# Kernel tuning notes

Hardware: AMD Instinct MI355X
Metric: run time of the kernel (lower is better)

## Reference

```python
import jax, jax.numpy as jnp
import numpy as np


def setup_inputs() -> dict:
    key = jax.random.key(0)
    ks = jax.random.split(key, 7)
    B, T, I, H, O = 128, 1024, 300, 128, 64
    s_ih = 1.0 / np.sqrt(H)
    return {
        "x": jax.random.normal(ks[0], (B, T, I), dtype=jnp.float32),
        "W_ih": jax.random.normal(ks[1], (4 * H, I), dtype=jnp.float32) * s_ih,
        "W_hh": jax.random.normal(ks[2], (4 * H, H), dtype=jnp.float32) * s_ih,
        "b_ih": jax.random.normal(ks[3], (4 * H,), dtype=jnp.float32) * s_ih,
        "b_hh": jax.random.normal(ks[4], (4 * H,), dtype=jnp.float32) * s_ih,
        "W1": jax.random.normal(ks[5], (O, H), dtype=jnp.float32) * s_ih,
        "b1": jax.random.normal(ks[6], (O,), dtype=jnp.float32) * s_ih,
    }


def reference(x, W_ih, W_hh, b_ih, b_hh, W1, b1):
    B, T, I = x.shape
    H = W_hh.shape[1]
    # Precompute the input-to-gate projections for all timesteps at once: [B,T,4H]
    x_gates = jnp.einsum("bti,gi->btg", x, W_ih) + b_ih + b_hh

    def step(carry, xg_t):
        h, c = carry
        gates = xg_t + h @ W_hh.T  # [B, 4H]
        i_g, f_g, g_g, o_g = jnp.split(gates, 4, axis=-1)
        i_g = jax.nn.sigmoid(i_g)
        f_g = jax.nn.sigmoid(f_g)
        g_g = jnp.tanh(g_g)
        o_g = jax.nn.sigmoid(o_g)
        c_new = f_g * c + i_g * g_g
        h_new = o_g * jnp.tanh(c_new)
        return (h_new, c_new), h_new

    h0 = jnp.zeros((B, H), dtype=x.dtype)
    c0 = jnp.zeros((B, H), dtype=x.dtype)
    _, all_h = jax.lax.scan(step, (h0, c0), jnp.swapaxes(x_gates, 0, 1))  # [T,B,H]
    h_seq = jnp.swapaxes(all_h, 0, 1)  # [B,T,H]
    # Dropout in eval mode (identity) for a deterministic reference.
    y = jnp.einsum("bth,oh->bto", h_seq, W1) + b1
    return y
```

## Files before the change

### kernel.cpp

```cpp
#include <hip/hip_runtime.h>
#include <hip/hip_fp16.h>

typedef __attribute__((ext_vector_type(8))) short  s16x8;
typedef __attribute__((ext_vector_type(4))) float  f32x4;
typedef __attribute__((ext_vector_type(4))) unsigned short u16x4;
typedef _Float16 f16x2 __attribute__((ext_vector_type(2)));
typedef _Float16 f16x8 __attribute__((ext_vector_type(8)));
typedef unsigned short u16;

#define MFMA16B(A, B, C) __builtin_amdgcn_mfma_f32_16x16x32_bf16((A), (B), (C), 0, 0, 0)
#define MFMA16H(A, B, C) __builtin_amdgcn_mfma_f32_16x16x32_f16((A), (B), (C), 0, 0, 0)

static __device__ __forceinline__ u16 f2bf(float f) {
    union { float f; unsigned u; } v; v.f = f;
    unsigned r = (v.u + 0x7fffu + ((v.u >> 16) & 1u)) >> 16;
    return (u16)r;
}

static __device__ __forceinline__ s16x8 pack_f16x8(float4 a, float4 b) {
    s16x8 r;
    r[0] = (short)__half_as_ushort(__float2half_rn(a.x));
    r[1] = (short)__half_as_ushort(__float2half_rn(a.y));
    r[2] = (short)__half_as_ushort(__float2half_rn(a.z));
    r[3] = (short)__half_as_ushort(__float2half_rn(a.w));
    r[4] = (short)__half_as_ushort(__float2half_rn(b.x));
    r[5] = (short)__half_as_ushort(__float2half_rn(b.y));
    r[6] = (short)__half_as_ushort(__float2half_rn(b.z));
    r[7] = (short)__half_as_ushort(__float2half_rn(b.w));
    return r;
}

static __device__ __forceinline__ float hu2f(u16 v) {
    __half_raw hr; hr.x = v; return __half2float(__half(hr));
}

static __device__ __forceinline__ float sigm(float x) {
    return __builtin_amdgcn_rcpf(1.f + __expf(-x));
}
static __device__ __forceinline__ float tanh_f(float x) {
    float e = __expf(-2.f * x);
    return fmaf(2.f, __builtin_amdgcn_rcpf(1.f + e), -1.f);
}

static __device__ __forceinline__ void wg_barrier() {
    asm volatile("s_waitcnt lgkmcnt(0)\n\ts_barrier" ::: "memory");
}

static __device__ __forceinline__ void lds_fence() {
    asm volatile("s_waitcnt lgkmcnt(0)" ::: "memory");
}

#define DPPB(v, ctrl) __builtin_bit_cast(float, __builtin_amdgcn_update_dpp(    \
        0, __builtin_bit_cast(int, (v)), (ctrl), 0xf, 0xf, true))

__global__ __launch_bounds__(256, 2)
void k1_gemm_xgates(const float* __restrict__ x, const float* __restrict__ W_ih,
                    const float* __restrict__ b_ih, const float* __restrict__ b_hh,
                    __half* __restrict__ xg) {
    const int n0 = blockIdx.x * 128;
    const int m0 = blockIdx.y * 128;
    const int tid = threadIdx.x;
    const int wave = tid >> 6, lane = tid & 63;
    const int lanelo = lane & 15, quad = lane >> 4;
    const int mw = (wave & 1) * 64, nw = (wave >> 1) * 64;

    __shared__ __align__(16) u16 As[128 * 40];
    __shared__ __align__(16) u16 Bs[128 * 40];

    f32x4 acc[4][4];
#pragma unroll
    for (int i = 0; i < 4; ++i)
#pragma unroll
        for (int j = 0; j < 4; ++j) acc[i][j] = (f32x4)0.f;

    const int srow = tid >> 1;
    const int scol = (tid & 1) * 16;
    const int grow = (srow & 3) * 128 + (n0 >> 2) + (srow >> 2);

    for (int kc = 0; kc < 10; ++kc) {
        const int k0 = kc * 32;
        const float* srcA = x + (size_t)(m0 + srow) * 300 + k0 + scol;
        const float* srcB = W_ih + (size_t)grow * 300 + k0 + scol;
        if (kc < 9) {
#pragma unroll
            for (int i = 0; i < 4; ++i) {
                const int col = scol + i * 4;
                float4 v = *(const float4*)(srcA + i * 4);
                u16x4 w; w.x = f2bf(v.x); w.y = f2bf(v.y); w.z = f2bf(v.z); w.w = f2bf(v.w);
                *(u16x4*)&As[srow * 40 + col] = w;
                float4 u = *(const float4*)(srcB + i * 4);
                u16x4 q; q.x = f2bf(u.x); q.y = f2bf(u.y); q.z = f2bf(u.z); q.w = f2bf(u.w);
                *(u16x4*)&Bs[srow * 40 + col] = q;
            }
        } else {
#pragma unroll
            for (int i = 0; i < 4; ++i) {
                const int col = scol + i * 4;
                float4 v = {0.f, 0.f, 0.f, 0.f}, u = {0.f, 0.f, 0.f, 0.f};
                if (k0 + col + 3 < 300) { v = *(const float4*)(srcA + i * 4);
                                          u = *(const float4*)(srcB + i * 4); }
                u16x4 w; w.x = f2bf(v.x); w.y = f2bf(v.y); w.z = f2bf(v.z); w.w = f2bf(v.w);
                *(u16x4*)&As[srow * 40 + col] = w;
                u16x4 q; q.x = f2bf(u.x); q.y = f2bf(u.y); q.z = f2bf(u.z); q.w = f2bf(u.w);
                *(u16x4*)&Bs[srow * 40 + col] = q;
            }
        }
        __syncthreads();

        s16x8 af[4], bf[4];
#pragma unroll
        for (int mt = 0; mt < 4; ++mt)
            af[mt] = *(const s16x8*)&As[(mw + mt * 16 + lanelo) * 40 + quad * 8];
#pragma unroll
        for (int nt = 0; nt < 4; ++nt)
            bf[nt] = *(const s16x8*)&Bs[(nw + nt * 16 + lanelo) * 40 + quad * 8];
#pragma unroll
        for (int mt = 0; mt < 4; ++mt)
#pragma unroll
            for (int nt = 0; nt < 4; ++nt)
                acc[mt][nt] = MFMA16B(af[mt], bf[nt], acc[mt][nt]);
        __syncthreads();
    }

#pragma unroll
    for (int nt = 0; nt < 4; ++nt) {
        const int n = n0 + nw + nt * 16 + lanelo;
        const int g = (n & 3) * 128 + (n >> 2);
        const float bs = b_ih[g] + b_hh[g];
#pragma unroll
        for (int mt = 0; mt < 4; ++mt) {
            const int mr = m0 + mw + mt * 16 + quad * 4;
#pragma unroll
            for (int r = 0; r < 4; ++r)
                xg[(size_t)(mr + r) * 512 + n] = __float2half(acc[mt][nt][r] + bs);
        }
    }
}

__global__ __launch_bounds__(512, 2)
void k2_lstm_rec(const __half* __restrict__ xg_all, const float* __restrict__ W_hh,
                 __half* __restrict__ h_seq) {
    const int b = blockIdx.x;
    const int tid = threadIdx.x;
    const int w = tid >> 6;
    const int l = tid & 63;
    const int col = 16 * w + (l >> 2);
    const int g = l & 3;
    const bool row0 = (l & 15) == 0;

    __shared__ __align__(16) u16  hbuf[2][128];
    __shared__ __align__(16) u16  zblk[104];
    __shared__ __align__(16) float gate_lds[512];

    f16x8 bfrag[4][4];
#pragma unroll
    for (int t = 0; t < 4; ++t)
#pragma unroll
        for (int ks = 0; ks < 4; ++ks) {
            const int n = 64 * w + 16 * t + (l & 15);
            const int grow = (n & 3) * 128 + (n >> 2);
            const float* p = W_hh + (size_t)grow * 128 + 32 * ks + (l >> 4) * 8;
            float4 v0 = *(const float4*)p;
            float4 v1 = *(const float4*)(p + 4);
            bfrag[t][ks] = __builtin_bit_cast(f16x8, pack_f16x8(v0, v1));
        }

    const float sb = (g == 2) ? 2.f : 1.f;
    const float bb = (g == 2) ? -1.f : 0.f;

    const u16* xp = (const u16*)xg_all + (size_t)b * 1024 * 512 + tid;
    u16 xa = xp[0];
    u16 xb = xp[512];

    if (tid < 128) hbuf[0][tid] = 0;
    if (tid < 104) zblk[tid] = 0;

    const u16* aA0 = row0 ? &hbuf[0][(l >> 4) * 8] : &zblk[0];
    const u16* aA1 = row0 ? &hbuf[1][(l >> 4) * 8] : &zblk[0];
    float* gw = &gate_lds[64 * w + l];
    const float* gr = &gate_lds[64 * w + l];

    float c = 0.f;
    __half* hout = h_seq + (size_t)b * 1024 * 128 + col;
    __syncthreads();

#define STEP(T, APTR, WB, XR, NXT) do {                                         \
        s16x8 _a0 = *(const s16x8*)(APTR);                                      \
        s16x8 _a1 = *(const s16x8*)(APTR + 32);                                 \
        s16x8 _a2 = *(const s16x8*)(APTR + 64);                                 \
        s16x8 _a3 = *(const s16x8*)(APTR + 96);                                 \
        f32x4 _ac0 = (f32x4)0.f, _ac1 = (f32x4)0.f;                             \
        f32x4 _ac2 = (f32x4)0.f, _ac3 = (f32x4)0.f;                             \
        f16x8 _af;                                                              \
        _af = __builtin_bit_cast(f16x8, _a0);                                   \
        _ac0 = MFMA16H(_af, bfrag[0][0], _ac0);                                 \
        _ac1 = MFMA16H(_af, bfrag[1][0], _ac1);                                 \
        _ac2 = MFMA16H(_af, bfrag[2][0], _ac2);                                 \
        _ac3 = MFMA16H(_af, bfrag[3][0], _ac3);                                 \
        _af = __builtin_bit_cast(f16x8, _a1);                                   \
        _ac0 = MFMA16H(_af, bfrag[0][1], _ac0);                                 \
        _ac1 = MFMA16H(_af, bfrag[1][1], _ac1);                                 \
        _ac2 = MFMA16H(_af, bfrag[2][1], _ac2);                                 \
        _ac3 = MFMA16H(_af, bfrag[3][1], _ac3);                                 \
        _af = __builtin_bit_cast(f16x8, _a2);                                   \
        _ac0 = MFMA16H(_af, bfrag[0][2], _ac0);                                 \
        _ac1 = MFMA16H(_af, bfrag[1][2], _ac1);                                 \
        _ac2 = MFMA16H(_af, bfrag[2][2], _ac2);                                 \
        _ac3 = MFMA16H(_af, bfrag[3][2], _ac3);                                 \
        _af = __builtin_bit_cast(f16x8, _a3);                                   \
        _ac0 = MFMA16H(_af, bfrag[0][3], _ac0);                                 \
        _ac1 = MFMA16H(_af, bfrag[1][3], _ac1);                                 \
        _ac2 = MFMA16H(_af, bfrag[2][3], _ac2);                                 \
        _ac3 = MFMA16H(_af, bfrag[3][3], _ac3);                                 \
        if (l < 16) {           \
            gw[0]  = _ac0[0];                                                   \
            gw[16] = _ac1[0];                                                   \
            gw[32] = _ac2[0];                                                   \
            gw[48] = _ac3[0];                                                   \
        }                                                                       \
        lds_fence();                        \
        const float _pre = *gr + hu2f(XR);                                      \
        XR = xp[(size_t)(NXT) * 512];                     \
        const float _act = fmaf(sb, sigm(sb * _pre), bb);                       \
        const float _ig = DPPB(_act, 0x00);                    \
        const float _fg = DPPB(_act, 0x55);                    \
        const float _gg = DPPB(_act, 0xAA);                    \
        const float _og = DPPB(_act, 0xFF);                    \
        c = fmaf(_fg, c, _ig * _gg);                                            \
        const float _hv = _og * tanh_f(c);                                      \
        const __half _hh = __float2half(_hv);                                   \
        if (g == 0) hbuf[WB][col] = (u16)__half_as_ushort(_hh);                 \
        if (g == 1) hout[(size_t)(T) * 128] = _hh;         \
        wg_barrier();                                         \
    } while (0)

    for (int t = 0; t < 1024; t += 2) {
        STEP(t,     aA0, 1, xa, (t + 2 < 1024 ? t + 2 : 1023));
        STEP(t + 1, aA1, 0, xb, (t + 3 < 1024 ? t + 3 : 1023));
    }
#undef STEP
}

__global__ __launch_bounds__(256, 2)
void k3_gemm_out(const u16* __restrict__ hseq, const float* __restrict__ W1,
                 const float* __restrict__ b1, float* __restrict__ y) {
    const int m0 = blockIdx.x * 128;
    const int tid = threadIdx.x;
    const int wave = tid >> 6, lane = tid & 63;
    const int lanelo = lane & 15, quad = lane >> 4;

    __shared__ __align__(16) u16 Ah[128 * 136];
    __shared__ __align__(16) u16 Bw[64 * 136];
    __shared__ float b1s[64];

    {
        const int row = tid >> 1, cg = (tid & 1) * 64;
        const u16* src = hseq + (size_t)(m0 + row) * 128 + cg;
#pragma unroll
        for (int i = 0; i < 8; ++i)
            *(s16x8*)&Ah[row * 136 + cg + i * 8] = *(const s16x8*)(src + i * 8);
    }
    {
        const int row = tid >> 2, cg = (tid & 3) * 32;
        const float* src = W1 + (size_t)row * 128 + cg;
#pragma unroll
        for (int i = 0; i < 4; ++i) {
            float4 v0 = *(const float4*)(src + i * 8);
            float4 v1 = *(const float4*)(src + i * 8 + 4);
            *(s16x8*)&Bw[row * 136 + cg + i * 8] = pack_f16x8(v0, v1);
        }
    }
    if (tid < 64) b1s[tid] = b1[tid];
    __syncthreads();

    f16x8 af[2][4], bf[4][4];
#pragma unroll
    for (int mt = 0; mt < 2; ++mt)
#pragma unroll
        for (int kt = 0; kt < 4; ++kt)
            af[mt][kt] = __builtin_bit_cast(f16x8,
                *(const s16x8*)&Ah[(wave * 32 + mt * 16 + lanelo) * 136 + kt * 32 + quad * 8]);
#pragma unroll
    for (int nt = 0; nt < 4; ++nt)
#pragma unroll
        for (int kt = 0; kt < 4; ++kt)
            bf[nt][kt] = __builtin_bit_cast(f16x8,
                *(const s16x8*)&Bw[(nt * 16 + lanelo) * 136 + kt * 32 + quad * 8]);

    f32x4 acc[2][4];
#pragma unroll
    for (int mt = 0; mt < 2; ++mt)
#pragma unroll
        for (int nt = 0; nt < 4; ++nt) acc[mt][nt] = (f32x4)0.f;
#pragma unroll
    for (int kt = 0; kt < 4; ++kt)
#pragma unroll
        for (int mt = 0; mt < 2; ++mt)
#pragma unroll
            for (int nt = 0; nt < 4; ++nt)
                acc[mt][nt] = MFMA16H(af[mt][kt], bf[nt][kt], acc[mt][nt]);

#pragma unroll
    for (int mt = 0; mt < 2; ++mt)
#pragma unroll
        for (int nt = 0; nt < 4; ++nt) {
            const int n = nt * 16 + lanelo;
            const float bs = b1s[n];
            const int mr = m0 + wave * 32 + mt * 16 + quad * 4;
#pragma unroll
            for (int r = 0; r < 4; ++r)
                y[(size_t)(mr + r) * 64 + n] = acc[mt][nt][r] + bs;
        }
}

extern "C" void kernel_launch(void* const* d_in, const int* in_sizes, int n_in,
                              void* d_out, int out_size, void* d_ws, size_t ws_size,
                              hipStream_t stream) {
    const float* x    = (const float*)d_in[0];
    const float* W_ih = (const float*)d_in[1];
    const float* W_hh = (const float*)d_in[2];
    const float* b_ih = (const float*)d_in[3];
    const float* b_hh = (const float*)d_in[4];
    const float* W1   = (const float*)d_in[5];
    const float* b1   = (const float*)d_in[6];
    float* y = (float*)d_out;

    const size_t XG_BYTES = (size_t)131072 * 512 * 2;
    const size_t HS_BYTES = (size_t)131072 * 128 * 2;
    if (ws_size < XG_BYTES + HS_BYTES) return;

    __half* xg   = (__half*)d_ws;
    __half* hseq = (__half*)((char*)d_ws + XG_BYTES);

    k1_gemm_xgates<<<dim3(4, 1024), 256, 0, stream>>>(x, W_ih, b_ih, b_hh, xg);
    k2_lstm_rec<<<128, 512, 0, stream>>>(xg, W_hh, hseq);
    k3_gemm_out<<<1024, 256, 0, stream>>>((const u16*)hseq, W1, b1, y);
}
```

Measured before the change: 884.9 us.

## Batch four sequences per LSTM recurrence block to fill MFMA rows

The recurrent kernel now processes four batch elements per workgroup instead of one. It uses four of the sixteen MFMA A-rows, where before only row zero was populated. The grid shrinks from 128 to 32 blocks and each step's elementwise gate math loops over four rows, with per-row cell state and prefetched x-gates. This amortizes the per-step MFMA, LDS exchange and barrier latency across more sequences, but leaves most CUs idle and lengthens the serial elementwise part of each step.

```diff
diff --git a/kernel.cpp b/kernel.cpp
--- a/kernel.cpp
+++ b/kernel.cpp
@@ -137,7 +137,7 @@
     }
 }
 
-__global__ __launch_bounds__(512, 2)
+__global__ __launch_bounds__(512, 1)
 void k2_lstm_rec(const __half* __restrict__ xg_all, const float* __restrict__ W_hh,
                  __half* __restrict__ h_seq) {
     const int b = blockIdx.x;
@@ -146,11 +146,12 @@
     const int l = tid & 63;
     const int col = 16 * w + (l >> 2);
     const int g = l & 3;
-    const bool row0 = (l & 15) == 0;
-
-    __shared__ __align__(16) u16  hbuf[2][128];
-    __shared__ __align__(16) u16  zblk[104];
-    __shared__ __align__(16) float gate_lds[512];
+    const int r_a = l & 15;
+    const int kg = l >> 4;
+
+    __shared__ __align__(16) u16   hbuf[2][4][136];
+    __shared__ __align__(16) u16   zblk[128];
+    __shared__ __align__(16) float gate_lds[8][64][4];
 
     f16x8 bfrag[4][4];
 #pragma unroll
@@ -168,27 +169,33 @@
     const float sb = (g == 2) ? 2.f : 1.f;
     const float bb = (g == 2) ? -1.f : 0.f;
 
-    const u16* xp = (const u16*)xg_all + (size_t)b * 1024 * 512 + tid;
-    u16 xa = xp[0];
-    u16 xb = xp[512];
-
-    if (tid < 128) hbuf[0][tid] = 0;
-    if (tid < 104) zblk[tid] = 0;
-
-    const u16* aA0 = row0 ? &hbuf[0][(l >> 4) * 8] : &zblk[0];
-    const u16* aA1 = row0 ? &hbuf[1][(l >> 4) * 8] : &zblk[0];
-    float* gw = &gate_lds[64 * w + l];
-    const float* gr = &gate_lds[64 * w + l];
-
-    float c = 0.f;
-    __half* hout = h_seq + (size_t)b * 1024 * 128 + col;
+    const u16* xp[4];
+    u16 xa[4], xb[4];
+    __half* hout[4];
+#pragma unroll
+    for (int r = 0; r < 4; ++r) {
+        xp[r] = (const u16*)xg_all + ((size_t)(4 * b + r) * 1024) * 512 + tid;
+        xa[r] = xp[r][0];
+        xb[r] = xp[r][512];
+        hout[r] = h_seq + (size_t)(4 * b + r) * 1024 * 128 + col;
+    }
+
+    if (tid < 272) ((unsigned*)&hbuf[0][0][0])[tid] = 0u;
+    if (tid < 64)  ((unsigned*)&zblk[0])[tid] = 0u;
+
+    const u16* aA[2];
+    aA[0] = (r_a < 4) ? &hbuf[0][r_a][kg * 8] : &zblk[kg * 8];
+    aA[1] = (r_a < 4) ? &hbuf[1][r_a][kg * 8] : &zblk[kg * 8];
+
+    float c[4] = {0.f, 0.f, 0.f, 0.f};
     __syncthreads();
 
-#define STEP(T, APTR, WB, XR, NXT) do {                                         \
-        s16x8 _a0 = *(const s16x8*)(APTR);                                      \
-        s16x8 _a1 = *(const s16x8*)(APTR + 32);                                 \
-        s16x8 _a2 = *(const s16x8*)(APTR + 64);                                 \
-        s16x8 _a3 = *(const s16x8*)(APTR + 96);                                 \
+#define STEP(T, RB, WB, XR, NXT) do {                                           \
+        const u16* _ap = aA[RB];                                                \
+        s16x8 _a0 = *(const s16x8*)(_ap);                                       \
+        s16x8 _a1 = *(const s16x8*)(_ap + 32);                                  \
+        s16x8 _a2 = *(const s16x8*)(_ap + 64);                                  \
+        s16x8 _a3 = *(const s16x8*)(_ap + 96);                                  \
         f32x4 _ac0 = (f32x4)0.f, _ac1 = (f32x4)0.f;                             \
         f32x4 _ac2 = (f32x4)0.f, _ac3 = (f32x4)0.f;                             \
         f16x8 _af;                                                              \
@@ -212,31 +219,35 @@
         _ac1 = MFMA16H(_af, bfrag[1][3], _ac1);                                 \
         _ac2 = MFMA16H(_af, bfrag[2][3], _ac2);                                 \
         _ac3 = MFMA16H(_af, bfrag[3][3], _ac3);                                 \
-        if (l < 16) {           \
-            gw[0]  = _ac0[0];                                                   \
-            gw[16] = _ac1[0];                                                   \
-            gw[32] = _ac2[0];                                                   \
-            gw[48] = _ac3[0];                                                   \
+        if (l < 16) {    \
+            *(f32x4*)&gate_lds[w][l][0]      = _ac0;                            \
+            *(f32x4*)&gate_lds[w][16 + l][0] = _ac1;                            \
+            *(f32x4*)&gate_lds[w][32 + l][0] = _ac2;                            \
+            *(f32x4*)&gate_lds[w][48 + l][0] = _ac3;                            \
         }                                                                       \
         lds_fence();                        \
-        const float _pre = *gr + hu2f(XR);                                      \
-        XR = xp[(size_t)(NXT) * 512];                     \
-        const float _act = fmaf(sb, sigm(sb * _pre), bb);                       \
-        const float _ig = DPPB(_act, 0x00);                    \
-        const float _fg = DPPB(_act, 0x55);                    \
-        const float _gg = DPPB(_act, 0xAA);                    \
-        const float _og = DPPB(_act, 0xFF);                    \
-        c = fmaf(_fg, c, _ig * _gg);                                            \
-        const float _hv = _og * tanh_f(c);                                      \
-        const __half _hh = __float2half(_hv);                                   \
-        if (g == 0) hbuf[WB][col] = (u16)__half_as_ushort(_hh);                 \
-        if (g == 1) hout[(size_t)(T) * 128] = _hh;         \
+        const f32x4 _g4 = *(const f32x4*)&gate_lds[w][l][0];                    \
+        _Pragma("unroll")                                                       \
+        for (int _r = 0; _r < 4; ++_r) {                                        \
+            const float _pre = _g4[_r] + hu2f(XR[_r]);                          \
+            XR[_r] = xp[_r][(size_t)(NXT) * 512];         \
+            const float _act = fmaf(sb, sigm(sb * _pre), bb);                   \
+            const float _ig = DPPB(_act, 0x00);                \
+            const float _fg = DPPB(_act, 0x55);                \
+            const float _gg = DPPB(_act, 0xAA);                \
+            const float _og = DPPB(_act, 0xFF);                \
+            c[_r] = fmaf(_fg, c[_r], _ig * _gg);                                \
+            const float _hv = _og * tanh_f(c[_r]);                              \
+            const __half _hh = __float2half(_hv);                               \
+            if (g == 0) hbuf[WB][_r][col] = (u16)__half_as_ushort(_hh);         \
+            if (g == 1) hout[_r][(size_t)(T) * 128] = _hh;       \
+        }                                                                       \
         wg_barrier();                                         \
     } while (0)
 
     for (int t = 0; t < 1024; t += 2) {
-        STEP(t,     aA0, 1, xa, (t + 2 < 1024 ? t + 2 : 1023));
-        STEP(t + 1, aA1, 0, xb, (t + 3 < 1024 ? t + 3 : 1023));
+        STEP(t,     0, 1, xa, (t + 2 < 1024 ? t + 2 : 1023));
+        STEP(t + 1, 1, 0, xb, (t + 3 < 1024 ? t + 3 : 1023));
     }
 #undef STEP
 }
@@ -333,6 +344,6 @@
     __half* hseq = (__half*)((char*)d_ws + XG_BYTES);
 
     k1_gemm_xgates<<<dim3(4, 1024), 256, 0, stream>>>(x, W_ih, b_ih, b_hh, xg);
-    k2_lstm_rec<<<128, 512, 0, stream>>>(xg, W_hh, hseq);
+    k2_lstm_rec<<<32, 512, 0, stream>>>(xg, W_hh, hseq);
     k3_gemm_out<<<1024, 256, 0, stream>>>((const u16*)hseq, W1, b1, y);
 }
```

Measured after the change: 2.541 ms. 187% more time.
